# Kernel tuning notes

Measured on AMD Instinct MI355X. Metric: run time of the kernel, lower is better.

The kernel has to match this reference:

```python
import jax, jax.numpy as jnp
import numpy as np

B, S, V, H = 16, 256, 32, 256
LN_EPS = 1e-5


def setup_inputs() -> dict:
    key = jax.random.key(0)
    ks = jax.random.split(key, 8)
    sW = 1.0 / np.sqrt(H)
    return {
        "x": jax.random.normal(ks[0], (B, S, V, 1), jnp.float32),
        "W1": jax.random.normal(ks[1], (V, H), jnp.float32),          # linear1: input_size=1
        "b1": jax.random.normal(ks[2], (V, H), jnp.float32) * 0.1,
        "W2": jax.random.normal(ks[3], (V, H, H), jnp.float32) * sW,
        "b2": jax.random.normal(ks[4], (V, H), jnp.float32) * 0.1,
        "Wg": jax.random.normal(ks[5], (V, H, H), jnp.float32) * sW,
        "bg": jax.random.normal(ks[6], (V, H), jnp.float32) * 0.1,
        "gamma": jnp.ones((V, H), jnp.float32),
        "beta": jnp.zeros((V, H), jnp.float32),
        "Wa": jax.random.normal(ks[7], (H,), jnp.float32) * sW,
        "ba": jnp.zeros((1,), jnp.float32),
    }


def reference(x, W1, b1, W2, b2, Wg, bg, gamma, beta, Wa, ba):
    # Batched GRN over all variables at once (replaces the per-var Python loop).
    # x: [B,S,V,1]; linear1 with input_size=1 is a scalar-vector outer product.
    h = jax.nn.relu(x * W1 + b1)                                  # [B,S,V,H]
    h = jnp.einsum('bsvh,vhk->bsvk', h, W2) + b2                  # linear2
    gated = jax.nn.sigmoid(jnp.einsum('bsvh,vhk->bsvk', h, Wg) + bg) * h
    # residual is the raw scalar input (last dim 1), broadcast over H as in torch
    pre = x + gated                                               # [B,S,V,H]
    mu = jnp.mean(pre, axis=-1, keepdims=True)
    var = jnp.mean(jnp.square(pre - mu), axis=-1, keepdims=True)
    var_outputs = (pre - mu) * jax.lax.rsqrt(var + LN_EPS) * gamma + beta
    # softmax attention pooling over variables
    scores = jnp.einsum('bsvh,h->bsv', var_outputs, Wa) + ba[0]   # [B,S,V]
    attn = jax.nn.softmax(scores, axis=-1)[..., None]             # [B,S,V,1]
    vsn_out = jnp.sum(var_outputs * attn, axis=2)                 # [B,S,H]
    return vsn_out, attn
```

## Files before the change

### kernel.cpp

```cpp
#include <hip/hip_runtime.h>
#include <hip/hip_bf16.h>

typedef _Float16 f16;
typedef _Float16 f16x2 __attribute__((ext_vector_type(2)));
typedef _Float16 f16x4 __attribute__((ext_vector_type(4)));
typedef _Float16 f16x8 __attribute__((ext_vector_type(8)));
typedef float f32x4 __attribute__((ext_vector_type(4)));

#define T_TOK 4096
#define V_N 32
#define H_N 256
#define LN_EPS_F 1e-5f
#define PADH 264

__device__ __forceinline__ void gload16(const f16* g, f16* l) {
    __builtin_amdgcn_global_load_lds(
        (const __attribute__((address_space(1))) void*)g,
        (__attribute__((address_space(3))) void*)l, 16, 0, 0);
}

__global__ __launch_bounds__(256) void prep_transpose(
    const float* __restrict__ W2, const float* __restrict__ Wg,
    f16* __restrict__ W2t, f16* __restrict__ Wgt)
{
    __shared__ float tile[64][65];
    int bid = blockIdx.x;
    int w = bid >> 9;
    int rem = bid & 511;
    int v = rem >> 4;
    int kt = (rem >> 2) & 3;
    int nt = rem & 3;
    const float* src = w ? Wg : W2;
    f16* dst = w ? Wgt : W2t;
    const float* base = src + ((size_t)v * H_N + (size_t)kt * 64) * H_N + nt * 64;
    int tid = threadIdx.x;
    #pragma unroll
    for (int p = 0; p < 16; ++p) {
        int idx = p * 256 + tid;
        int r = idx >> 6, c = idx & 63;
        tile[r][c] = base[(size_t)r * H_N + c];
    }
    __syncthreads();
    f16* obase = dst + ((size_t)v * H_N + (size_t)nt * 64) * H_N + kt * 64;
    #pragma unroll
    for (int p = 0; p < 16; ++p) {
        int idx = p * 256 + tid;
        int r = idx >> 6, c = idx & 63;
        obase[(size_t)r * H_N + c] = (f16)tile[c][r];
    }
}

__global__ __launch_bounds__(512, 2) void fused_grn(
    const float* __restrict__ x,
    const float* __restrict__ W1, const float* __restrict__ b1,
    const f16* __restrict__ W2t, const float* __restrict__ b2,
    const f16* __restrict__ Wgt, const float* __restrict__ bg,
    const float* __restrict__ gamma, const float* __restrict__ beta,
    const float* __restrict__ Wa, const float* __restrict__ ba,
    f16* __restrict__ VO,
    float* __restrict__ scores)
{
    __shared__ f16 Hs[128][PADH];
    __shared__ f16 Bb[2][256 * 64];

    int bid = blockIdx.x;
    int xcd = bid & 7, r = bid >> 3;
    int v  = (xcd << 2) + (r >> 5);
    int mt = r & 31;
    int m0 = mt * 128;

    int tid = threadIdx.x;
    int wid = tid >> 6, lane = tid & 63;
    int wr = wid >> 2, wc = wid & 3;
    int lo = lane & 15, hi = lane >> 4;

    const f16* BW2 = W2t + (size_t)v * (H_N * H_N);
    const f16* BWg = Wgt + (size_t)v * (H_N * H_N);

    auto stage = [&](const f16* B, int kk0, int buf) {
        #pragma unroll
        for (int i = 0; i < 4; ++i) {
            int rsub = lane >> 3;
            int rr = (wid << 5) + (i << 3) + rsub;
            int cs = (lane & 7) ^ rsub;
            gload16(B + (size_t)rr * H_N + kk0 + cs * 8,
                    &Bb[buf][(wid << 11) + (i << 9)]);
        }
    };

    f32x4 acc[4][4] = {};
    const f32x4 zero4 = {0.f, 0.f, 0.f, 0.f};

#define GEMM_STEP(BUF, KT)                                                         \
    {                                                                              \
        _Pragma("unroll")                                                          \
        for (int ks = 0; ks < 2; ++ks) {                                           \
            f16x8 af[4], bf[4];                                                    \
            _Pragma("unroll")                                                      \
            for (int rb = 0; rb < 4; ++rb)                                         \
                af[rb] = *(const f16x8*)&Hs[wr * 64 + rb * 16 + lo]                \
                                           [(KT) * 64 + ks * 32 + hi * 8];         \
            _Pragma("unroll")                                                      \
            for (int cb = 0; cb < 4; ++cb) {                                       \
                int n = wc * 64 + cb * 16 + lo;                                    \
                int ch = (ks * 4 + hi) ^ (lo & 7);                                 \
                bf[cb] = *(const f16x8*)&Bb[BUF][n * 64 + ch * 8];                 \
            }                                                                      \
            _Pragma("unroll")                                                      \
            for (int rb = 0; rb < 4; ++rb)                                         \
                _Pragma("unroll")                                                  \
                for (int cb = 0; cb < 4; ++cb)                                     \
                    acc[rb][cb] = __builtin_amdgcn_mfma_f32_16x16x32_f16(          \
                        af[rb], bf[cb], acc[rb][cb], 0, 0, 0);                     \
        }                                                                          \
    }

    stage(BW2, 0, 0);
    {
        int r0 = tid >> 3;
        int kg = tid & 7;
        const float* W1v = W1 + v * H_N;
        const float* b1v = b1 + v * H_N;
        float xv0 = x[(size_t)(m0 + r0) * V_N + v];
        float xv1 = x[(size_t)(m0 + r0 + 64) * V_N + v];
        #pragma unroll
        for (int kt = 0; kt < 4; ++kt) {
            int k0 = kt * 64 + kg * 8;
            f16x8 a0, a1;
            #pragma unroll
            for (int j = 0; j < 8; ++j) {
                float w = W1v[k0 + j], b = b1v[k0 + j];
                float h0 = fmaf(xv0, w, b);
                float h1 = fmaf(xv1, w, b);
                a0[j] = (f16)(h0 > 0.f ? h0 : 0.f);
                a1[j] = (f16)(h1 > 0.f ? h1 : 0.f);
            }
            *(f16x8*)&Hs[r0][k0] = a0;
            *(f16x8*)&Hs[r0 + 64][k0] = a1;
        }
    }
    __syncthreads();

    #pragma unroll
    for (int kt = 0; kt < 4; ++kt) {
        if (kt < 3) stage(BW2, (kt + 1) * 64, (kt + 1) & 1);
        else        stage(BWg, 0, 0);
        GEMM_STEP(kt & 1, kt)
        __syncthreads();
    }

    #pragma unroll
    for (int cb = 0; cb < 4; ++cb) {
        int n = wc * 64 + cb * 16 + lo;
        float bias = b2[v * H_N + n];
        #pragma unroll
        for (int rb = 0; rb < 4; ++rb) {
            #pragma unroll
            for (int reg = 0; reg < 4; ++reg) {
                int m = wr * 64 + rb * 16 + hi * 4 + reg;
                Hs[m][n] = (f16)(acc[rb][cb][reg] + bias);
                acc[rb][cb][reg] = 0.f;
            }
        }
    }
    __syncthreads();

    #pragma unroll
    for (int kt = 0; kt < 4; ++kt) {
        if (kt < 3) stage(BWg, (kt + 1) * 64, (kt + 1) & 1);
        GEMM_STEP(kt & 1, kt)
        __syncthreads();
    }

    #pragma unroll
    for (int cb = 0; cb < 4; ++cb) {
        int n = wc * 64 + cb * 16 + lo;
        float bias = bg[v * H_N + n];
        #pragma unroll
        for (int rb = 0; rb < 4; ++rb) {
            #pragma unroll
            for (int reg = 0; reg < 4; ++reg) {
                int m = wr * 64 + rb * 16 + hi * 4 + reg;
                float a = acc[rb][cb][reg] + bias;
                float g = 1.f / (1.f + __expf(-a));
                float h2v = (float)Hs[m][n];
                Hs[m][n] = (f16)(g * h2v);
            }
        }
    }
    __syncthreads();

    {
        f32x4 gm = *(const f32x4*)&gamma[v * H_N + lane * 4];
        f32x4 bt = *(const f32x4*)&beta[v * H_N + lane * 4];
        f32x4 wa = *(const f32x4*)&Wa[lane * 4];
        float bav = ba[0];
        #pragma unroll
        for (int i = 0; i < 16; ++i) {
            int row = (wid << 4) + i;
            f16x4 gv = *(const f16x4*)&Hs[row][lane * 4];
            float g0 = gv[0], g1 = gv[1], g2 = gv[2], g3 = gv[3];
            float s = g0 + g1 + g2 + g3;
            float q = g0 * g0 + g1 * g1 + g2 * g2 + g3 * g3;
            #pragma unroll
            for (int mm = 1; mm < 64; mm <<= 1) {
                s += __shfl_xor(s, mm, 64);
                q += __shfl_xor(q, mm, 64);
            }
            float mu = s * (1.f / 256.f);
            float var = q * (1.f / 256.f) - mu * mu;
            float inv = rsqrtf(var + LN_EPS_F);
            float o0 = (g0 - mu) * inv * gm[0] + bt[0];
            float o1 = (g1 - mu) * inv * gm[1] + bt[1];
            float o2 = (g2 - mu) * inv * gm[2] + bt[2];
            float o3 = (g3 - mu) * inv * gm[3] + bt[3];
            f16x4 ov = { (f16)o0, (f16)o1, (f16)o2, (f16)o3 };
            *(f16x4*)&VO[((size_t)v * T_TOK + m0 + row) * H_N + lane * 4] = ov;
            float sp = o0 * wa[0] + o1 * wa[1] + o2 * wa[2] + o3 * wa[3];
            #pragma unroll
            for (int mm = 1; mm < 64; mm <<= 1) sp += __shfl_xor(sp, mm, 64);
            if (lane == 0) scores[(size_t)(m0 + row) * V_N + v] = sp + bav;
        }
    }
#undef GEMM_STEP
}

__global__ __launch_bounds__(128) void pool(
    const f16* __restrict__ VO,
    const float* __restrict__ scores,
    float* __restrict__ out)
{
    int t = blockIdx.x, tid = threadIdx.x;
    __shared__ float sc[V_N];
    if (tid < V_N) sc[tid] = scores[t * V_N + tid];
    __syncthreads();
    float mx = -1e30f;
    #pragma unroll
    for (int v = 0; v < V_N; ++v) mx = fmaxf(mx, sc[v]);
    float e[V_N];
    float sum = 0.f;
    #pragma unroll
    for (int v = 0; v < V_N; ++v) { e[v] = __expf(sc[v] - mx); sum += e[v]; }
    float isum = 1.f / sum;
    float a0 = 0.f, a1 = 0.f;
    #pragma unroll
    for (int v = 0; v < V_N; ++v) {
        f16x2 vv = *(const f16x2*)&VO[((size_t)v * T_TOK + t) * H_N + tid * 2];
        float w = e[v] * isum;
        a0 = fmaf((float)vv[0], w, a0);
        a1 = fmaf((float)vv[1], w, a1);
    }
    *(float2*)&out[(size_t)t * H_N + tid * 2] = make_float2(a0, a1);
    if (tid < V_N)
        out[(size_t)T_TOK * H_N + (size_t)t * V_N + tid] = e[tid] * isum;
}

extern "C" void kernel_launch(void* const* d_in, const int* in_sizes, int n_in,
                              void* d_out, int out_size, void* d_ws, size_t ws_size,
                              hipStream_t stream)
{
    const float* x     = (const float*)d_in[0];
    const float* W1    = (const float*)d_in[1];
    const float* b1    = (const float*)d_in[2];
    const float* W2    = (const float*)d_in[3];
    const float* b2    = (const float*)d_in[4];
    const float* Wg    = (const float*)d_in[5];
    const float* bg    = (const float*)d_in[6];
    const float* gamma = (const float*)d_in[7];
    const float* beta  = (const float*)d_in[8];
    const float* Wa    = (const float*)d_in[9];
    const float* ba    = (const float*)d_in[10];
    float* out = (float*)d_out;

    char* ws = (char*)d_ws;
    f16* W2t = (f16*)ws;
    f16* Wgt = (f16*)(ws + ((size_t)4 << 20));
    f16* VO  = (f16*)(ws + ((size_t)8 << 20));
    float* scores = (float*)(ws + ((size_t)72 << 20));

    prep_transpose<<<1024, 256, 0, stream>>>(W2, Wg, W2t, Wgt);
    fused_grn<<<1024, 512, 0, stream>>>(x, W1, b1, W2t, b2, Wgt, bg,
                                        gamma, beta, Wa, ba, VO, scores);
    pool<<<4096, 128, 0, stream>>>(VO, scores, out);
}
```

Before: 122.1 us.

## Rewrite GRN kernel as register-resident per-wave GEMM without LDS staging

The fused GRN kernel no longer stages weights and activations in shared memory. Each wave now owns 16 tokens and computes the whole 256-wide output in registers, reading weight fragments straight from global/L2. The layer-1 output is moved into the second GEMM's operand layout with cross-lane shuffles, and LayerNorm reductions are done in registers. A small prep kernel converts W1/b1 to fp16 so linear1 runs in half precision. This removes LDS traffic and barriers but re-reads the per-variable weights from cache for every wave, and the fp16 linear1 costs some precision.

Result: slower. 308.8 us (+153.0%).

```diff
diff --git a/kernel.cpp b/kernel.cpp
--- a/kernel.cpp
+++ b/kernel.cpp
@@ -11,13 +11,9 @@
 #define V_N 32
 #define H_N 256
 #define LN_EPS_F 1e-5f
-#define PADH 264
-
-__device__ __forceinline__ void gload16(const f16* g, f16* l) {
-    __builtin_amdgcn_global_load_lds(
-        (const __attribute__((address_space(1))) void*)g,
-        (__attribute__((address_space(3))) void*)l, 16, 0, 0);
-}
+
+union U4 { f16x4 h; int i[2]; };
+union U8 { f16x8 h; int i[4]; };
 
 __global__ __launch_bounds__(256) void prep_transpose(
     const float* __restrict__ W2, const float* __restrict__ Wg,
@@ -50,9 +46,18 @@
     }
 }
 
-__global__ __launch_bounds__(512, 2) void fused_grn(
+__global__ __launch_bounds__(256) void prep_w1(
+    const float* __restrict__ W1, const float* __restrict__ b1,
+    f16* __restrict__ W1h, f16* __restrict__ b1h)
+{
+    int i = blockIdx.x * 256 + threadIdx.x;
+    W1h[i] = (f16)W1[i];
+    b1h[i] = (f16)b1[i];
+}
+
+__global__ __launch_bounds__(256) void fused_grn(
     const float* __restrict__ x,
-    const float* __restrict__ W1, const float* __restrict__ b1,
+    const f16* __restrict__ W1h, const f16* __restrict__ b1h,
     const f16* __restrict__ W2t, const float* __restrict__ b2,
     const f16* __restrict__ Wgt, const float* __restrict__ bg,
     const float* __restrict__ gamma, const float* __restrict__ beta,
@@ -60,169 +65,112 @@
     f16* __restrict__ VO,
     float* __restrict__ scores)
 {
-    __shared__ f16 Hs[128][PADH];
-    __shared__ f16 Bb[2][256 * 64];
-
     int bid = blockIdx.x;
-    int xcd = bid & 7, r = bid >> 3;
-    int v  = (xcd << 2) + (r >> 5);
-    int mt = r & 31;
-    int m0 = mt * 128;
-
+    int xcd = bid & 7, rr = bid >> 3;
+    int v  = (xcd << 2) + (rr >> 6);
+    int mt = rr & 63;
     int tid = threadIdx.x;
-    int wid = tid >> 6, lane = tid & 63;
-    int wr = wid >> 2, wc = wid & 3;
+    int w = tid >> 6, lane = tid & 63;
     int lo = lane & 15, hi = lane >> 4;
-
-    const f16* BW2 = W2t + (size_t)v * (H_N * H_N);
-    const f16* BWg = Wgt + (size_t)v * (H_N * H_N);
-
-    auto stage = [&](const f16* B, int kk0, int buf) {
-        #pragma unroll
-        for (int i = 0; i < 4; ++i) {
-            int rsub = lane >> 3;
-            int rr = (wid << 5) + (i << 3) + rsub;
-            int cs = (lane & 7) ^ rsub;
-            gload16(B + (size_t)rr * H_N + kk0 + cs * 8,
-                    &Bb[buf][(wid << 11) + (i << 9)]);
-        }
-    };
-
-    f32x4 acc[4][4] = {};
-    const f32x4 zero4 = {0.f, 0.f, 0.f, 0.f};
-
-#define GEMM_STEP(BUF, KT)                                                         \
-    {                                                                              \
-        _Pragma("unroll")                                                          \
-        for (int ks = 0; ks < 2; ++ks) {                                           \
-            f16x8 af[4], bf[4];                                                    \
-            _Pragma("unroll")                                                      \
-            for (int rb = 0; rb < 4; ++rb)                                         \
-                af[rb] = *(const f16x8*)&Hs[wr * 64 + rb * 16 + lo]                \
-                                           [(KT) * 64 + ks * 32 + hi * 8];         \
-            _Pragma("unroll")                                                      \
-            for (int cb = 0; cb < 4; ++cb) {                                       \
-                int n = wc * 64 + cb * 16 + lo;                                    \
-                int ch = (ks * 4 + hi) ^ (lo & 7);                                 \
-                bf[cb] = *(const f16x8*)&Bb[BUF][n * 64 + ch * 8];                 \
-            }                                                                      \
-            _Pragma("unroll")                                                      \
-            for (int rb = 0; rb < 4; ++rb)                                         \
-                _Pragma("unroll")                                                  \
-                for (int cb = 0; cb < 4; ++cb)                                     \
-                    acc[rb][cb] = __builtin_amdgcn_mfma_f32_16x16x32_f16(          \
-                        af[rb], bf[cb], acc[rb][cb], 0, 0, 0);                     \
-        }                                                                          \
-    }
-
-    stage(BW2, 0, 0);
-    {
-        int r0 = tid >> 3;
-        int kg = tid & 7;
-        const float* W1v = W1 + v * H_N;
-        const float* b1v = b1 + v * H_N;
-        float xv0 = x[(size_t)(m0 + r0) * V_N + v];
-        float xv1 = x[(size_t)(m0 + r0 + 64) * V_N + v];
-        #pragma unroll
-        for (int kt = 0; kt < 4; ++kt) {
-            int k0 = kt * 64 + kg * 8;
-            f16x8 a0, a1;
-            #pragma unroll
-            for (int j = 0; j < 8; ++j) {
-                float w = W1v[k0 + j], b = b1v[k0 + j];
-                float h0 = fmaf(xv0, w, b);
-                float h1 = fmaf(xv1, w, b);
-                a0[j] = (f16)(h0 > 0.f ? h0 : 0.f);
-                a1[j] = (f16)(h1 > 0.f ? h1 : 0.f);
-            }
-            *(f16x8*)&Hs[r0][k0] = a0;
-            *(f16x8*)&Hs[r0 + 64][k0] = a1;
-        }
-    }
-    __syncthreads();
-
-    #pragma unroll
-    for (int kt = 0; kt < 4; ++kt) {
-        if (kt < 3) stage(BW2, (kt + 1) * 64, (kt + 1) & 1);
-        else        stage(BWg, 0, 0);
-        GEMM_STEP(kt & 1, kt)
-        __syncthreads();
-    }
-
-    #pragma unroll
-    for (int cb = 0; cb < 4; ++cb) {
-        int n = wc * 64 + cb * 16 + lo;
-        float bias = b2[v * H_N + n];
-        #pragma unroll
-        for (int rb = 0; rb < 4; ++rb) {
-            #pragma unroll
-            for (int reg = 0; reg < 4; ++reg) {
-                int m = wr * 64 + rb * 16 + hi * 4 + reg;
-                Hs[m][n] = (f16)(acc[rb][cb][reg] + bias);
-                acc[rb][cb][reg] = 0.f;
-            }
-        }
-    }
-    __syncthreads();
-
-    #pragma unroll
-    for (int kt = 0; kt < 4; ++kt) {
-        if (kt < 3) stage(BWg, (kt + 1) * 64, (kt + 1) & 1);
-        GEMM_STEP(kt & 1, kt)
-        __syncthreads();
-    }
-
-    #pragma unroll
-    for (int cb = 0; cb < 4; ++cb) {
-        int n = wc * 64 + cb * 16 + lo;
-        float bias = bg[v * H_N + n];
-        #pragma unroll
-        for (int rb = 0; rb < 4; ++rb) {
-            #pragma unroll
-            for (int reg = 0; reg < 4; ++reg) {
-                int m = wr * 64 + rb * 16 + hi * 4 + reg;
-                float a = acc[rb][cb][reg] + bias;
-                float g = 1.f / (1.f + __expf(-a));
-                float h2v = (float)Hs[m][n];
-                Hs[m][n] = (f16)(g * h2v);
-            }
-        }
-    }
-    __syncthreads();
-
-    {
-        f32x4 gm = *(const f32x4*)&gamma[v * H_N + lane * 4];
-        f32x4 bt = *(const f32x4*)&beta[v * H_N + lane * 4];
-        f32x4 wa = *(const f32x4*)&Wa[lane * 4];
-        float bav = ba[0];
-        #pragma unroll
-        for (int i = 0; i < 16; ++i) {
-            int row = (wid << 4) + i;
-            f16x4 gv = *(const f16x4*)&Hs[row][lane * 4];
-            float g0 = gv[0], g1 = gv[1], g2 = gv[2], g3 = gv[3];
-            float s = g0 + g1 + g2 + g3;
-            float q = g0 * g0 + g1 * g1 + g2 * g2 + g3 * g3;
-            #pragma unroll
-            for (int mm = 1; mm < 64; mm <<= 1) {
-                s += __shfl_xor(s, mm, 64);
-                q += __shfl_xor(q, mm, 64);
-            }
-            float mu = s * (1.f / 256.f);
-            float var = q * (1.f / 256.f) - mu * mu;
-            float inv = rsqrtf(var + LN_EPS_F);
-            float o0 = (g0 - mu) * inv * gm[0] + bt[0];
-            float o1 = (g1 - mu) * inv * gm[1] + bt[1];
-            float o2 = (g2 - mu) * inv * gm[2] + bt[2];
-            float o3 = (g3 - mu) * inv * gm[3] + bt[3];
-            f16x4 ov = { (f16)o0, (f16)o1, (f16)o2, (f16)o3 };
-            *(f16x4*)&VO[((size_t)v * T_TOK + m0 + row) * H_N + lane * 4] = ov;
-            float sp = o0 * wa[0] + o1 * wa[1] + o2 * wa[2] + o3 * wa[3];
-            #pragma unroll
-            for (int mm = 1; mm < 64; mm <<= 1) sp += __shfl_xor(sp, mm, 64);
-            if (lane == 0) scores[(size_t)(m0 + row) * V_N + v] = sp + bav;
-        }
-    }
-#undef GEMM_STEP
+    int m = mt * 64 + w * 16 + lo;
+
+    const f16* W2v = W2t + ((size_t)v << 16);
+    const f16* Wgv = Wgt + ((size_t)v << 16);
+
+    float xs = x[(size_t)m * V_N + v];
+    f16 xh = (f16)xs;
+    f16x8 x8 = { xh, xh, xh, xh, xh, xh, xh, xh };
+
+    f32x4 acc[16] = {};
+
+    #pragma unroll
+    for (int kt = 0; kt < 8; ++kt) {
+        const int k0 = kt * 32 + hi * 8;
+        f16x8 w8 = *(const f16x8*)&W1h[v * H_N + k0];
+        f16x8 c8 = *(const f16x8*)&b1h[v * H_N + k0];
+        f16x8 hv = x8 * w8 + c8;
+        #pragma unroll
+        for (int j = 0; j < 8; ++j) hv[j] = hv[j] > (f16)0 ? hv[j] : (f16)0;
+        #pragma unroll
+        for (int nf = 0; nf < 16; ++nf) {
+            f16x8 af = *(const f16x8*)&W2v[(size_t)((nf * 16 + lo) << 8) + k0];
+            acc[nf] = __builtin_amdgcn_mfma_f32_16x16x32_f16(af, hv, acc[nf], 0, 0, 0);
+        }
+    }
+
+    int H2p[16][2];
+    #pragma unroll
+    for (int nf = 0; nf < 16; ++nf) {
+        f32x4 b4 = *(const f32x4*)&b2[v * H_N + nf * 16 + hi * 4];
+        f32x4 h = acc[nf] + b4;
+        U4 u; u.h = f16x4{ (f16)h[0], (f16)h[1], (f16)h[2], (f16)h[3] };
+        H2p[nf][0] = u.i[0]; H2p[nf][1] = u.i[1];
+        acc[nf] = f32x4{0.f, 0.f, 0.f, 0.f};
+    }
+
+    int iq0 = lo + ((((hi << 1))     & 3) << 4);
+    int iq1 = lo + ((((hi << 1) | 1) & 3) << 4);
+    bool hiB = (hi >> 1) != 0;
+    #pragma unroll
+    for (int kt = 0; kt < 8; ++kt) {
+        int A0 = H2p[2 * kt][0],     A1 = H2p[2 * kt][1];
+        int B0 = H2p[2 * kt + 1][0], B1 = H2p[2 * kt + 1][1];
+        int a0 = __shfl(A0, iq0), a1 = __shfl(A1, iq0);
+        int a2 = __shfl(A0, iq1), a3 = __shfl(A1, iq1);
+        int b0 = __shfl(B0, iq0), b1_ = __shfl(B1, iq0);
+        int b2_ = __shfl(B0, iq1), b3 = __shfl(B1, iq1);
+        U8 u;
+        u.i[0] = hiB ? b0  : a0;
+        u.i[1] = hiB ? b1_ : a1;
+        u.i[2] = hiB ? b2_ : a2;
+        u.i[3] = hiB ? b3  : a3;
+        const int k0 = kt * 32 + hi * 8;
+        #pragma unroll
+        for (int nf = 0; nf < 16; ++nf) {
+            f16x8 af = *(const f16x8*)&Wgv[(size_t)((nf * 16 + lo) << 8) + k0];
+            acc[nf] = __builtin_amdgcn_mfma_f32_16x16x32_f16(af, u.h, acc[nf], 0, 0, 0);
+        }
+    }
+
+    float s = 0.f, q = 0.f;
+    #pragma unroll
+    for (int nf = 0; nf < 16; ++nf) {
+        f32x4 bgv = *(const f32x4*)&bg[v * H_N + nf * 16 + hi * 4];
+        U4 u; u.i[0] = H2p[nf][0]; u.i[1] = H2p[nf][1];
+        #pragma unroll
+        for (int r = 0; r < 4; ++r) {
+            float a = acc[nf][r] + bgv[r];
+            float g = 1.f / (1.f + __expf(-a));
+            float val = g * (float)u.h[r];
+            acc[nf][r] = val;
+            s += val; q += val * val;
+        }
+    }
+    s += __shfl_xor(s, 16); s += __shfl_xor(s, 32);
+    q += __shfl_xor(q, 16); q += __shfl_xor(q, 32);
+    float mu  = s * (1.f / 256.f);
+    float var = q * (1.f / 256.f) - mu * mu;
+    float inv = rsqrtf(var + LN_EPS_F);
+
+    float sp = 0.f;
+    f16* VOr = VO + ((size_t)v * T_TOK + m) * H_N;
+    #pragma unroll
+    for (int nf = 0; nf < 16; ++nf) {
+        int n0 = nf * 16 + hi * 4;
+        f32x4 gm = *(const f32x4*)&gamma[v * H_N + n0];
+        f32x4 bt = *(const f32x4*)&beta[v * H_N + n0];
+        f32x4 wa = *(const f32x4*)&Wa[n0];
+        f16x4 ov;
+        #pragma unroll
+        for (int r = 0; r < 4; ++r) {
+            float o = (acc[nf][r] - mu) * inv * gm[r] + bt[r];
+            sp += o * wa[r];
+            ov[r] = (f16)o;
+        }
+        *(f16x4*)&VOr[n0] = ov;
+    }
+    sp += __shfl_xor(sp, 16); sp += __shfl_xor(sp, 32);
+    if (hi == 0) scores[(size_t)m * V_N + v] = sp + ba[0];
 }
 
 __global__ __launch_bounds__(128) void pool(
@@ -246,9 +194,9 @@
     #pragma unroll
     for (int v = 0; v < V_N; ++v) {
         f16x2 vv = *(const f16x2*)&VO[((size_t)v * T_TOK + t) * H_N + tid * 2];
-        float w = e[v] * isum;
-        a0 = fmaf((float)vv[0], w, a0);
-        a1 = fmaf((float)vv[1], w, a1);
+        float ww = e[v] * isum;
+        a0 = fmaf((float)vv[0], ww, a0);
+        a1 = fmaf((float)vv[1], ww, a1);
     }
     *(float2*)&out[(size_t)t * H_N + tid * 2] = make_float2(a0, a1);
     if (tid < V_N)
@@ -277,9 +225,12 @@
     f16* Wgt = (f16*)(ws + ((size_t)4 << 20));
     f16* VO  = (f16*)(ws + ((size_t)8 << 20));
     float* scores = (float*)(ws + ((size_t)72 << 20));
+    f16* W1h = (f16*)(ws + ((size_t)72 << 20) + (512 << 10));
+    f16* b1h = (f16*)(ws + ((size_t)72 << 20) + (528 << 10));
 
     prep_transpose<<<1024, 256, 0, stream>>>(W2, Wg, W2t, Wgt);
-    fused_grn<<<1024, 512, 0, stream>>>(x, W1, b1, W2t, b2, Wgt, bg,
+    prep_w1<<<32, 256, 0, stream>>>(W1, b1, W1h, b1h);
+    fused_grn<<<2048, 256, 0, stream>>>(x, W1h, b1h, W2t, b2, Wgt, bg,
                                         gamma, beta, Wa, ba, VO, scores);
     pool<<<4096, 128, 0, stream>>>(VO, scores, out);
 }
```
